# Kernel tuning notes

Measured on AMD Instinct MI355X. Metric: run time of the kernel, lower is better.

## Reference

```python
import jax, jax.numpy as jnp
import numpy as np
import math

D_MODEL = 512

def setup_inputs() -> dict:
    key = jax.random.key(0)
    k1, k2, k3 = jax.random.split(key, 3)
    X = jax.random.normal(k1, (4, 8192, D_MODEL), dtype=jnp.float32)
    # nn.Linear(d, d, bias=False) weights, applied as x @ W.T
    s = 1.0 / math.sqrt(D_MODEL)
    W_v = jax.random.uniform(k2, (D_MODEL, D_MODEL), dtype=jnp.float32, minval=-s, maxval=s)
    W_theta = jax.random.uniform(k3, (D_MODEL, D_MODEL), dtype=jnp.float32, minval=-s, maxval=s)
    return {"X": X, "W_v": W_v, "W_theta": W_theta}

def reference(X, W_v, W_theta):
    # X: [B, n, d]
    n = X.shape[1]
    d = X.shape[2]
    XW_v = X @ W_v.T            # [B, n, d]
    theta_X = X @ W_theta.T     # [B, n, d]
    # first term: (1/n) * ones(n,n) @ XW_v == column mean broadcast over rows
    first_term = jnp.mean(XW_v, axis=1, keepdims=True)  # [B, 1, d], broadcasts
    # second term: (1/(n*sqrt(d))) * (X @ theta_X^T) @ XW_v
    # associativity-reduced: theta_X^T @ XW_v is [B, d, d]
    kv = jnp.einsum('bnd,bne->bde', theta_X, XW_v)       # [B, d, d]
    second_term = (X @ kv) / (n * math.sqrt(d))          # [B, n, d]
    return first_term + second_term
```

## Files before the change

kernel.cpp:

```cpp
#include <hip/hip_runtime.h>
#include <stdint.h>


typedef __bf16 bf16x8 __attribute__((ext_vector_type(8)));
typedef float f32x4 __attribute__((ext_vector_type(4)));
typedef unsigned short u16x4 __attribute__((ext_vector_type(4)));
typedef unsigned short u16x8 __attribute__((ext_vector_type(8)));
typedef unsigned int u32x2 __attribute__((ext_vector_type(2)));

#define BK 32

#define BAR asm volatile("s_barrier" ::: "memory")

template <int N>
__device__ __forceinline__ void vmw() {
  static_assert(N == 0 || N == 1 || N == 2 || N == 4 || N == 8, "vmw");
  if constexpr (N == 0) asm volatile("s_waitcnt vmcnt(0)" ::: "memory");
  else if constexpr (N == 1) asm volatile("s_waitcnt vmcnt(1)" ::: "memory");
  else if constexpr (N == 2) asm volatile("s_waitcnt vmcnt(2)" ::: "memory");
  else if constexpr (N == 4) asm volatile("s_waitcnt vmcnt(4)" ::: "memory");
  else if constexpr (N == 8) asm volatile("s_waitcnt vmcnt(8)" ::: "memory");
}

__device__ __forceinline__ unsigned short f2bf(float f) {
  union { float f; unsigned int u; } c; c.f = f;
  unsigned int u = c.u;
  return (unsigned short)((u + 0x7FFFu + ((u >> 16) & 1u)) >> 16);
}
__device__ __forceinline__ float bf2f(unsigned short h) {
  union { unsigned int u; float f; } c; c.u = ((unsigned int)h) << 16;
  return c.f;
}

__device__ __forceinline__ void gld16(const void* g, void* l) {
  using gptr_t = const __attribute__((address_space(1))) void*;
  using lptr_t = __attribute__((address_space(3))) void*;
  __builtin_amdgcn_global_load_lds((gptr_t)(uintptr_t)g,
                                   (lptr_t)(uint32_t)(uintptr_t)l, 16, 0, 0);
}

template <int TB>
__device__ __forceinline__ void gemm_tile(const unsigned short* __restrict__ A, int lda,
                                          const unsigned short* __restrict__ B, int ldb,
                                          int m0, int n0, f32x4 (&acc)[TB / 32][TB / 32]) {
  static_assert(TB == 64 || TB == 128, "TB");
  constexpr int FR = TB / 32;
  constexpr int LJ = (TB * 4) / 256;
  constexpr int LPS = 2 * LJ;
  constexpr int NK = 512 / BK;
  __shared__ unsigned short sA[3][TB * BK];
  __shared__ unsigned short sB[3][TB * BK];
  const int tid = threadIdx.x;
  const int lane = tid & 63;
  const int w = tid >> 6;
  const int wm = w >> 1, wn = w & 1;
  const int quad = lane >> 4, l16 = lane & 15;
  const int sq = (quad ^ ((l16 >> 1) & 3)) * 8;

#pragma unroll
  for (int mi = 0; mi < FR; mi++)
#pragma unroll
    for (int ni = 0; ni < FR; ni++) acc[mi][ni] = f32x4{0.f, 0.f, 0.f, 0.f};

  auto stage = [&](int bb, int kt) {
    const int kk = kt * BK;
#pragma unroll
    for (int j = 0; j < LJ; j++) {
      const int slot = w * (LJ * 64) + j * 64 + lane;
      const int row = slot >> 2;
      const int col = ((slot & 3) ^ ((slot >> 3) & 3)) * 8;
      const int basegr = w * (LJ * 64) + j * 64;
      gld16(A + (size_t)(m0 + row) * lda + kk + col, (char*)sA[bb] + (size_t)basegr * 16);
      gld16(B + (size_t)(n0 + row) * ldb + kk + col, (char*)sB[bb] + (size_t)basegr * 16);
    }
  };

  auto compute = [&](int bb) {
    const unsigned short* as = sA[bb];
    const unsigned short* bs = sB[bb];
    bf16x8 af[FR], bfr[FR];
#pragma unroll
    for (int mi = 0; mi < FR; mi++)
      af[mi] = *(const bf16x8*)&as[(wm * (TB / 2) + mi * 16 + l16) * BK + sq];
#pragma unroll
    for (int ni = 0; ni < FR; ni++)
      bfr[ni] = *(const bf16x8*)&bs[(wn * (TB / 2) + ni * 16 + l16) * BK + sq];
    __builtin_amdgcn_s_setprio(1);
#pragma unroll
    for (int mi = 0; mi < FR; mi++)
#pragma unroll
      for (int ni = 0; ni < FR; ni++)
        acc[mi][ni] = __builtin_amdgcn_mfma_f32_16x16x32_bf16(af[mi], bfr[ni],
                                                              acc[mi][ni], 0, 0, 0);
    __builtin_amdgcn_s_setprio(0);
  };

  stage(0, 0);
  stage(1, 1);
  stage(2, 2);
#pragma unroll
  for (int kt = 0; kt < NK; ++kt) {
    if (kt < NK - 2) { vmw<2 * LPS>(); }
    else if (kt == NK - 2) { vmw<LPS>(); }
    else { vmw<0>(); }
    BAR;
    compute(kt % 3);
    BAR;
    if (kt < NK - 3) stage(kt % 3, kt + 3);
  }
}

__device__ __forceinline__ void gemm_tile_nt(const unsigned short* __restrict__ Xs,
                                             int m0, int n0, f32x4 (&acc)[4][4]) {
  constexpr int LPS = 4;
  constexpr int NK = 16;
  __shared__ unsigned short sA[3][128 * BK];
  __shared__ unsigned short sB[3][128 * BK];
  const int tid = threadIdx.x;
  const int lane = tid & 63;
  const int w = tid >> 6;
  const int wm = w >> 1, wn = w & 1;
  const int quad = lane >> 4, l16 = lane & 15;

#pragma unroll
  for (int mi = 0; mi < 4; mi++)
#pragma unroll
    for (int ni = 0; ni < 4; ni++) acc[mi][ni] = f32x4{0.f, 0.f, 0.f, 0.f};

  auto stage = [&](int bb, int kt) {
#pragma unroll
    for (int j = 0; j < 2; j++) {
      const int g = w * 128 + j * 64 + lane;
      const int dblk = g >> 6;
      const int nblk = (g >> 3) & 7;
      const int nr = (g >> 1) & 3;
      const int half = g & 1;
      const int n = kt * 32 + nblk * 4 + nr;
      const int base = w * 128 + j * 64;
      gld16(Xs + (size_t)n * 512 + m0 + dblk * 16 + half * 8,
            (char*)sA[bb] + (size_t)base * 16);
      gld16(Xs + (size_t)n * 512 + n0 + dblk * 16 + half * 8,
            (char*)sB[bb] + (size_t)base * 16);
    }
  };

  auto compute = [&](int bb) {
    const unsigned int abase =
        (unsigned int)(uintptr_t)(&sA[bb][0]) + (unsigned int)(quad * 256 + l16 * 8);
    const unsigned int bbase =
        (unsigned int)(uintptr_t)(&sB[bb][0]) + (unsigned int)(quad * 256 + l16 * 8);
    u32x2 ra[4][2], rb[4][2];
#pragma unroll
    for (int mi = 0; mi < 4; mi++) {
      const unsigned int pa = abase + (unsigned int)((wm * 4 + mi) * 1024);
      asm volatile("ds_read_b64_tr_b16 %0, %1" : "=v"(ra[mi][0]) : "v"(pa));
      asm volatile("ds_read_b64_tr_b16 %0, %1 offset:128" : "=v"(ra[mi][1]) : "v"(pa));
    }
#pragma unroll
    for (int ni = 0; ni < 4; ni++) {
      const unsigned int pb = bbase + (unsigned int)((wn * 4 + ni) * 1024);
      asm volatile("ds_read_b64_tr_b16 %0, %1" : "=v"(rb[ni][0]) : "v"(pb));
      asm volatile("ds_read_b64_tr_b16 %0, %1 offset:128" : "=v"(rb[ni][1]) : "v"(pb));
    }
    asm volatile("s_waitcnt lgkmcnt(0)" ::: "memory");
    __builtin_amdgcn_sched_barrier(0);
    union U { unsigned int u[4]; bf16x8 v; };
    bf16x8 af[4], bfr[4];
#pragma unroll
    for (int mi = 0; mi < 4; mi++) {
      U ua;
      ua.u[0] = ra[mi][0][0]; ua.u[1] = ra[mi][0][1];
      ua.u[2] = ra[mi][1][0]; ua.u[3] = ra[mi][1][1];
      af[mi] = ua.v;
    }
#pragma unroll
    for (int ni = 0; ni < 4; ni++) {
      U ub;
      ub.u[0] = rb[ni][0][0]; ub.u[1] = rb[ni][0][1];
      ub.u[2] = rb[ni][1][0]; ub.u[3] = rb[ni][1][1];
      bfr[ni] = ub.v;
    }
    __builtin_amdgcn_s_setprio(1);
#pragma unroll
    for (int mi = 0; mi < 4; mi++)
#pragma unroll
      for (int ni = 0; ni < 4; ni++)
        acc[mi][ni] = __builtin_amdgcn_mfma_f32_16x16x32_bf16(af[mi], bfr[ni],
                                                              acc[mi][ni], 0, 0, 0);
    __builtin_amdgcn_s_setprio(0);
  };

  stage(0, 0);
  stage(1, 1);
  stage(2, 2);
#pragma unroll
  for (int kt = 0; kt < NK; ++kt) {
    if (kt < NK - 2) { vmw<2 * LPS>(); }
    else if (kt == NK - 2) { vmw<LPS>(); }
    else { vmw<0>(); }
    BAR;
    compute(kt % 3);
    BAR;
    if (kt < NK - 3) stage(kt % 3, kt + 3);
  }
}

__global__ __launch_bounds__(256) void prep_kernel(const float* __restrict__ X,
                                                   unsigned short* __restrict__ Xb) {
  const int t = threadIdx.x;
  const size_t base = (size_t)blockIdx.x * 8192;
  f32x4 v[8];
#pragma unroll
  for (int k = 0; k < 4; k++) {
    const size_t idx = base + (size_t)k * 2048 + (size_t)t * 8;
    v[2 * k] = *(const f32x4*)(X + idx);
    v[2 * k + 1] = *(const f32x4*)(X + idx + 4);
  }
  __builtin_amdgcn_sched_barrier(0);
#pragma unroll
  for (int k = 0; k < 4; k++) {
    const size_t idx = base + (size_t)k * 2048 + (size_t)t * 8;
    u16x8 o;
#pragma unroll
    for (int j = 0; j < 4; j++) o[j] = f2bf(v[2 * k][j]);
#pragma unroll
    for (int j = 0; j < 4; j++) o[4 + j] = f2bf(v[2 * k + 1][j]);
    *(u16x8*)(Xb + idx) = o;
  }
}

__global__ __launch_bounds__(256) void prep_w_kernel(const float* __restrict__ Wv,
                                                     const float* __restrict__ Wth,
                                                     unsigned short* __restrict__ Wvb,
                                                     unsigned short* __restrict__ Wtb,
                                                     float* __restrict__ mean_x) {
  const int blk = blockIdx.x;
  const int t = threadIdx.x;
  if (blk == 0) {
#pragma unroll
    for (int i = 0; i < 8; i++) mean_x[t + i * 256] = 0.f;
  }
  const float* src = (blk < 128) ? Wv : Wth;
  unsigned short* dst = (blk < 128) ? Wvb : Wtb;
  const int i = (blk & 127) * 256 + t;
  const f32x4* pp = (const f32x4*)(src + (size_t)i * 8);
  f32x4 v0 = pp[0], v1 = pp[1];
  u16x8 o;
  o[0] = f2bf(v0[0]); o[1] = f2bf(v0[1]); o[2] = f2bf(v0[2]); o[3] = f2bf(v0[3]);
  o[4] = f2bf(v1[0]); o[5] = f2bf(v1[1]); o[6] = f2bf(v1[2]); o[7] = f2bf(v1[3]);
  *(u16x8*)(dst + (size_t)i * 8) = o;
}

static __device__ const int TI[10] = {0, 0, 0, 0, 1, 1, 1, 2, 2, 3};
static __device__ const int TJ[10] = {0, 1, 2, 3, 1, 2, 3, 2, 3, 3};

__global__ __launch_bounds__(256) void g_gemm_kernel(const unsigned short* __restrict__ Xb,
                                                     float* __restrict__ G_part,
                                                     float* __restrict__ mean_x) {
  const int t = blockIdx.y;
  const int z = blockIdx.x;
  const int b = z >> 4, s = z & 15;
  const unsigned short* Xs = Xb + (size_t)(b * 8192 + s * 512) * 512;
  if (t == 10) {
    const int w = threadIdx.x >> 6, l = threadIdx.x & 63;
    float cs[8] = {0.f, 0.f, 0.f, 0.f, 0.f, 0.f, 0.f, 0.f};
    for (int i0 = 0; i0 < 128; i0 += 8) {
      u16x8 val[8];
#pragma unroll
      for (int i = 0; i < 8; i++) {
        const int r = w + 4 * (i0 + i);
        val[i] = *(const u16x8*)(Xs + (size_t)r * 512 + l * 8);
      }
      __builtin_amdgcn_sched_barrier(0);
#pragma unroll
      for (int i = 0; i < 8; i++)
#pragma unroll
        for (int j = 0; j < 8; j++) cs[j] += bf2f(val[i][j]);
    }
#pragma unroll
    for (int j = 0; j < 8; j++)
      atomicAdd(&mean_x[b * 512 + l * 8 + j], cs[j]);
    return;
  }
  const int m0 = TI[t] * 128, n0 = TJ[t] * 128;
  f32x4 acc[4][4];
  gemm_tile_nt(Xs, m0, n0, acc);
  float* Cp = G_part + ((size_t)z * 10 + t) * 16384;
  const int tid = threadIdx.x, lane = tid & 63, w = tid >> 6;
  const int wm = w >> 1, wn = w & 1, quad = lane >> 4, l16 = lane & 15;
#pragma unroll
  for (int mi = 0; mi < 4; mi++)
#pragma unroll
    for (int ni = 0; ni < 4; ni++) {
      const int ml = wm * 64 + mi * 16 + quad * 4;
      const int nl = wn * 64 + ni * 16 + l16;
      *(f32x4*)(Cp + (size_t)nl * 128 + ml) = acc[mi][ni];
    }
}

__global__ __launch_bounds__(256) void g_fin_kernel(const float* __restrict__ G_part,
                                                    unsigned short* __restrict__ Gb,
                                                    const float* __restrict__ mean_x,
                                                    const float* __restrict__ Wv,
                                                    float* __restrict__ meanV) {
  const int blk = blockIdx.x;
  if (blk >= 320) {
    const int idx = (blk - 320) * 256 + threadIdx.x;
    const int b = idx >> 9, e = idx & 511;
    const float* mx = mean_x + b * 512;
    const float* wr = Wv + (size_t)e * 512;
    float s = 0.f;
    for (int d = 0; d < 512; d += 4) {
      f32x4 a = *(const f32x4*)(mx + d);
      f32x4 w4 = *(const f32x4*)(wr + d);
      s += a[0] * w4[0] + a[1] * w4[1] + a[2] * w4[2] + a[3] * w4[3];
    }
    meanV[idx] = s * (1.f / 8192.f);
    return;
  }
  const int b = blk / 80, rem = blk % 80;
  const int t = rem >> 3, cc = rem & 7;
  const int i = TI[t], j = TJ[t];
  const int m0 = i * 128, n0 = j * 128;
  const int tid = threadIdx.x;
  const int np = cc * 16 + (tid >> 4);
  const int mp = (tid & 15) * 8;
  f32x4 s0 = f32x4{0.f, 0.f, 0.f, 0.f}, s1 = f32x4{0.f, 0.f, 0.f, 0.f};
#pragma unroll
  for (int s = 0; s < 16; s++) {
    const float* p = G_part + (((size_t)(b * 16 + s)) * 10 + t) * 16384 + (size_t)np * 128 + mp;
    s0 += *(const f32x4*)p;
    s1 += *(const f32x4*)(p + 4);
  }
  const float scale = (float)(1.0 / (8192.0 * 22.627416997969522));
  unsigned short h[8];
#pragma unroll
  for (int r = 0; r < 4; r++) { h[r] = f2bf(s0[r] * scale); h[r + 4] = f2bf(s1[r] * scale); }
  unsigned short* Gbb = Gb + (size_t)b * 262144;
#pragma unroll
  for (int r = 0; r < 8; r++)
    Gbb[(size_t)(m0 + mp + r) * 512 + (n0 + np)] = h[r];
  if (i != j) {
    u16x8 o;
#pragma unroll
    for (int r = 0; r < 8; r++) o[r] = h[r];
    *(u16x8*)(Gbb + (size_t)(n0 + np) * 512 + (m0 + mp)) = o;
  }
}

__global__ __launch_bounds__(256) void gemm_rm_kernel(const unsigned short* __restrict__ A,
                                                      const unsigned short* __restrict__ B,
                                                      unsigned short* __restrict__ C,
                                                      size_t Abs, size_t Bbs) {
  const int b = blockIdx.z;
  const int m0 = blockIdx.x * 64, n0 = blockIdx.y * 64;
  f32x4 acc[2][2];
  gemm_tile<64>(A + (size_t)b * Abs, 512, B + (size_t)b * Bbs, 512, m0, n0, acc);
  unsigned short* Cb = C + (size_t)b * 262144;
  const int tid = threadIdx.x, lane = tid & 63, w = tid >> 6;
  const int wm = w >> 1, wn = w & 1, quad = lane >> 4, l16 = lane & 15;
#pragma unroll
  for (int mi = 0; mi < 2; mi++)
#pragma unroll
    for (int ni = 0; ni < 2; ni++) {
      const int m = m0 + wm * 32 + mi * 16 + quad * 4;
      const int n = n0 + wn * 32 + ni * 16 + l16;
#pragma unroll
      for (int r = 0; r < 4; r++)
        Cb[(size_t)(m + r) * 512 + n] = f2bf(acc[mi][ni][r]);
    }
}

__global__ __launch_bounds__(256) void gemm_out_kernel(
    const unsigned short* __restrict__ Xb, const unsigned short* __restrict__ kvt,
    const float* __restrict__ meanV, float* __restrict__ out) {
  const int D = blockIdx.x;
  const int gm = (D & 7) + ((D >> 5) << 3);
  const int nt = (D >> 3) & 3;
  const int m0 = gm * 128, n0 = nt * 128;
  const int b = gm >> 6;
  const unsigned short* Bm = kvt + (size_t)b * 262144;
  f32x4 acc[4][4];
  gemm_tile<128>(Xb, 512, Bm, 512, m0, n0, acc);
  const int tid = threadIdx.x, lane = tid & 63, w = tid >> 6;
  const int wm = w >> 1, wn = w & 1, quad = lane >> 4, l16 = lane & 15;
#pragma unroll
  for (int ni = 0; ni < 4; ni++) {
    const int e = n0 + wn * 64 + ni * 16 + l16;
    const float mu = meanV[b * 512 + e];
#pragma unroll
    for (int mi = 0; mi < 4; mi++) {
      const int m = m0 + wm * 64 + mi * 16 + quad * 4;
#pragma unroll
      for (int r = 0; r < 4; r++)
        out[(size_t)(m + r) * 512 + e] = acc[mi][ni][r] + mu;
    }
  }
}

extern "C" void kernel_launch(void* const* d_in, const int* in_sizes, int n_in,
                              void* d_out, int out_size, void* d_ws, size_t ws_size,
                              hipStream_t stream) {
  const float* X = (const float*)d_in[0];
  const float* Wv = (const float*)d_in[1];
  const float* Wth = (const float*)d_in[2];
  float* out = (float*)d_out;
  char* ws = (char*)d_ws;

  unsigned short* Xb = (unsigned short*)(ws);
  float* G_part = (float*)(ws + 67108864ull);
  unsigned short* Gb = (unsigned short*)(ws + 109051904ull);
  unsigned short* Ht = (unsigned short*)(ws + 111149056ull);
  unsigned short* kvt = (unsigned short*)(ws + 113246208ull);
  unsigned short* Wvb = (unsigned short*)(ws + 115343360ull);
  unsigned short* Wtb = (unsigned short*)(ws + 115867648ull);
  float* mean_x = (float*)(ws + 116391936ull);
  float* meanV = (float*)(ws + 116400128ull);

  prep_w_kernel<<<256, 256, 0, stream>>>(Wv, Wth, Wvb, Wtb, mean_x);
  prep_kernel<<<2048, 256, 0, stream>>>(X, Xb);

  g_gemm_kernel<<<dim3(64, 11), 256, 0, stream>>>(Xb, G_part, mean_x);
  g_fin_kernel<<<328, 256, 0, stream>>>(G_part, Gb, mean_x, Wv, meanV);

  gemm_rm_kernel<<<dim3(8, 8, 4), 256, 0, stream>>>(Wvb, Gb, Ht, 0, 262144);
  gemm_rm_kernel<<<dim3(8, 8, 4), 256, 0, stream>>>(Ht, Wtb, kvt, 262144, 0);

  gemm_out_kernel<<<1024, 256, 0, stream>>>(Xb, kvt, meanV, out);
}
```

Before: 219.1 us.

## Switch GEMM tiles to double-buffered LDS and merge weight/X prep kernels

Both GEMM tile routines drop from a three-stage to a two-stage shared-memory pipeline, which cuts LDS use per block and may allow more resident blocks, but leaves less prefetch depth to hide load latency. Separately, the weight-conversion kernel is folded into the X-conversion kernel as extra blocks, removing one kernel launch and its gap.

New measurement: 220.7 us. Within noise of the previous version (+0.7%).

```diff
diff --git a/kernel.cpp b/kernel.cpp
--- a/kernel.cpp
+++ b/kernel.cpp
@@ -48,8 +48,8 @@
   constexpr int LJ = (TB * 4) / 256;
   constexpr int LPS = 2 * LJ;
   constexpr int NK = 512 / BK;
-  __shared__ unsigned short sA[3][TB * BK];
-  __shared__ unsigned short sB[3][TB * BK];
+  __shared__ unsigned short sA[2][TB * BK];
+  __shared__ unsigned short sB[2][TB * BK];
   const int tid = threadIdx.x;
   const int lane = tid & 63;
   const int w = tid >> 6;
@@ -97,16 +97,13 @@
 
   stage(0, 0);
   stage(1, 1);
-  stage(2, 2);
 #pragma unroll
   for (int kt = 0; kt < NK; ++kt) {
-    if (kt < NK - 2) { vmw<2 * LPS>(); }
-    else if (kt == NK - 2) { vmw<LPS>(); }
-    else { vmw<0>(); }
+    if (kt < NK - 1) { vmw<LPS>(); } else { vmw<0>(); }
     BAR;
-    compute(kt % 3);
+    compute(kt & 1);
     BAR;
-    if (kt < NK - 3) stage(kt % 3, kt + 3);
+    if (kt + 2 < NK) stage(kt & 1, kt + 2);
   }
 }
 
@@ -114,8 +111,8 @@
                                              int m0, int n0, f32x4 (&acc)[4][4]) {
   constexpr int LPS = 4;
   constexpr int NK = 16;
-  __shared__ unsigned short sA[3][128 * BK];
-  __shared__ unsigned short sB[3][128 * BK];
+  __shared__ unsigned short sA[2][128 * BK];
+  __shared__ unsigned short sB[2][128 * BK];
   const int tid = threadIdx.x;
   const int lane = tid & 63;
   const int w = tid >> 6;
@@ -192,23 +189,43 @@
 
   stage(0, 0);
   stage(1, 1);
-  stage(2, 2);
 #pragma unroll
   for (int kt = 0; kt < NK; ++kt) {
-    if (kt < NK - 2) { vmw<2 * LPS>(); }
-    else if (kt == NK - 2) { vmw<LPS>(); }
-    else { vmw<0>(); }
+    if (kt < NK - 1) { vmw<LPS>(); } else { vmw<0>(); }
     BAR;
-    compute(kt % 3);
+    compute(kt & 1);
     BAR;
-    if (kt < NK - 3) stage(kt % 3, kt + 3);
+    if (kt + 2 < NK) stage(kt & 1, kt + 2);
   }
 }
 
 __global__ __launch_bounds__(256) void prep_kernel(const float* __restrict__ X,
-                                                   unsigned short* __restrict__ Xb) {
+                                                   unsigned short* __restrict__ Xb,
+                                                   const float* __restrict__ Wv,
+                                                   const float* __restrict__ Wth,
+                                                   unsigned short* __restrict__ Wvb,
+                                                   unsigned short* __restrict__ Wtb,
+                                                   float* __restrict__ mean_x) {
   const int t = threadIdx.x;
-  const size_t base = (size_t)blockIdx.x * 8192;
+  const int bid = blockIdx.x;
+  if (bid >= 2048) {
+    const int blk = bid - 2048;
+    if (blk == 0) {
+#pragma unroll
+      for (int i = 0; i < 8; i++) mean_x[t + i * 256] = 0.f;
+    }
+    const float* src = (blk < 128) ? Wv : Wth;
+    unsigned short* dst = (blk < 128) ? Wvb : Wtb;
+    const int i = (blk & 127) * 256 + t;
+    const f32x4* pp = (const f32x4*)(src + (size_t)i * 8);
+    f32x4 v0 = pp[0], v1 = pp[1];
+    u16x8 o;
+    o[0] = f2bf(v0[0]); o[1] = f2bf(v0[1]); o[2] = f2bf(v0[2]); o[3] = f2bf(v0[3]);
+    o[4] = f2bf(v1[0]); o[5] = f2bf(v1[1]); o[6] = f2bf(v1[2]); o[7] = f2bf(v1[3]);
+    *(u16x8*)(dst + (size_t)i * 8) = o;
+    return;
+  }
+  const size_t base = (size_t)bid * 8192;
   f32x4 v[8];
 #pragma unroll
   for (int k = 0; k < 4; k++) {
@@ -227,28 +244,6 @@
     for (int j = 0; j < 4; j++) o[4 + j] = f2bf(v[2 * k + 1][j]);
     *(u16x8*)(Xb + idx) = o;
   }
-}
-
-__global__ __launch_bounds__(256) void prep_w_kernel(const float* __restrict__ Wv,
-                                                     const float* __restrict__ Wth,
-                                                     unsigned short* __restrict__ Wvb,
-                                                     unsigned short* __restrict__ Wtb,
-                                                     float* __restrict__ mean_x) {
-  const int blk = blockIdx.x;
-  const int t = threadIdx.x;
-  if (blk == 0) {
-#pragma unroll
-    for (int i = 0; i < 8; i++) mean_x[t + i * 256] = 0.f;
-  }
-  const float* src = (blk < 128) ? Wv : Wth;
-  unsigned short* dst = (blk < 128) ? Wvb : Wtb;
-  const int i = (blk & 127) * 256 + t;
-  const f32x4* pp = (const f32x4*)(src + (size_t)i * 8);
-  f32x4 v0 = pp[0], v1 = pp[1];
-  u16x8 o;
-  o[0] = f2bf(v0[0]); o[1] = f2bf(v0[1]); o[2] = f2bf(v0[2]); o[3] = f2bf(v0[3]);
-  o[4] = f2bf(v1[0]); o[5] = f2bf(v1[1]); o[6] = f2bf(v1[2]); o[7] = f2bf(v1[3]);
-  *(u16x8*)(dst + (size_t)i * 8) = o;
 }
 
 static __device__ const int TI[10] = {0, 0, 0, 0, 1, 1, 1, 2, 2, 3};
@@ -417,8 +412,7 @@
   float* mean_x = (float*)(ws + 116391936ull);
   float* meanV = (float*)(ws + 116400128ull);
 
-  prep_w_kernel<<<256, 256, 0, stream>>>(Wv, Wth, Wvb, Wtb, mean_x);
-  prep_kernel<<<2048, 256, 0, stream>>>(X, Xb);
+  prep_kernel<<<2304, 256, 0, stream>>>(X, Xb, Wv, Wth, Wvb, Wtb, mean_x);
 
   g_gemm_kernel<<<dim3(64, 11), 256, 0, stream>>>(Xb, G_part, mean_x);
   g_fin_kernel<<<328, 256, 0, stream>>>(G_part, Gb, mean_x, Wv, meanV);
```
